# Optimization experiments

Measured on AMD Instinct MI355X. Metric: run time of the kernel, lower is better.

The kernel has to match this reference:

```python
import jax, jax.numpy as jnp
import numpy as np

N = 100000          # num nodes
E = 1600000         # num edges (before self loops)
IN_C = 128
OUT_C = 64
RATIO = 0.5
NEG_SLOPE = 0.2


def setup_inputs() -> dict:
    key = jax.random.key(0)
    k1, k2, k3, k4, k5 = jax.random.split(key, 5)
    x = jax.random.normal(k1, (N, IN_C), jnp.float32)
    # edges with no self loops (module removes then re-adds self loops)
    src = jax.random.randint(k2, (E,), 0, N, dtype=jnp.int32)
    off = jax.random.randint(k3, (E,), 1, N, dtype=jnp.int32)
    tgt = (src + off) % N
    edge_index = jnp.stack([src, tgt])  # [2, E], row0=source(j), row1=target(i)
    # glorot init
    s_w = float(np.sqrt(6.0 / (IN_C + OUT_C)))
    weight = jax.random.uniform(k4, (IN_C, OUT_C), jnp.float32, -s_w, s_w)
    s_a = float(np.sqrt(6.0 / (1 + 2 * OUT_C)))
    att = jax.random.uniform(k5, (1, 2 * OUT_C), jnp.float32, -s_a, s_a)
    batch = jnp.zeros((N,), jnp.int32)  # single graph
    return {"x": x, "weight": weight, "att": att,
            "edge_index": edge_index, "batch": batch, "bn": 0}


def reference(x, weight, att, edge_index, batch, bn):
    # add self loops (static shapes: E + N edges)
    loops = jnp.arange(N, dtype=edge_index.dtype)
    src = jnp.concatenate([edge_index[0], loops])  # edge_index_j (source)
    tgt = jnp.concatenate([edge_index[1], loops])  # edge_index_i (target)

    h = x @ weight                      # [N, OUT_C]
    x_j = h[src]                        # [E+N, OUT_C] gathered source feats
    x_i = h[tgt]

    # alpha = (cat([x_i, x_j]) * att).sum(-1)
    alpha = x_i @ att[0, :OUT_C] + x_j @ att[0, OUT_C:]   # [E+N]
    alpha = jnp.where(alpha > 0, alpha, NEG_SLOPE * alpha)  # leaky_relu

    # edge-softmax grouped by target node (every node has a self loop -> no empty segment)
    m = jax.ops.segment_max(alpha, tgt, num_segments=N)
    a = jnp.exp(alpha - m[tgt])
    denom = jax.ops.segment_sum(a, tgt, num_segments=N)
    alpha = a / (denom[tgt] + 1e-16)

    # node importance = sum of attention over outgoing edges (grouped by source)
    alpha_sum = jax.ops.segment_sum(alpha, src, num_segments=N)

    # topk node selection (ratio of all nodes; single graph)
    k = int(np.ceil(RATIO * N))
    _, topk_idx = jax.lax.top_k(alpha_sum, k)
    node_mask = jnp.zeros((N,), bool).at[topk_idx].set(True)

    # filter_dn: keep edges whose both endpoints survive; mask instead of compacting
    edge_mask = node_mask[src] & node_mask[tgt]
    alpha_m = jnp.where(edge_mask, alpha, 0.0)

    # weighted scatter-add aggregation to target nodes (aggr='add')
    out = jax.ops.segment_sum(alpha_m[:, None] * x_j, tgt, num_segments=N)  # [N, OUT_C]
    # bn flag is 0 -> BatchNorm skipped
    return out, edge_mask, node_mask
```

## Files before the change

kernel.cpp:

```cpp
#include <hip/hip_runtime.h>
#include <stdint.h>

#define IN_C 128
#define OUT_C 64
#define NEG_SLOPE 0.2f
#define RB 256
#define RBINS 512
#define STAGE 8192
#define SXP 260
#define NGH (RBINS * RB)
#define NGHS (RBINS * RBINS)

typedef unsigned int u32;
typedef unsigned long long u64;

__device__ __forceinline__ u32 fenc(float f) {
  u32 u = __float_as_uint(f);
  return (u & 0x80000000u) ? ~u : (u | 0x80000000u);
}
__device__ __forceinline__ u64 key64(float v, int i) {
  return (((u64)fenc(v)) << 32) | (u64)(0xffffffffu - (u32)i);
}

__global__ __launch_bounds__(256) void k_init(u32* hist8, u32* done, u32* sel, u32* cnt, u32 k) {
  int i = blockIdx.x * 256 + threadIdx.x;
  if (i < 2048) hist8[i] = 0u;
  if (i < 8) { done[i] = 0u; cnt[i] = 0u; }
  if (i == 0) { sel[0] = 0u; sel[1] = 0u; sel[2] = k; sel[3] = 0u; }
}

__global__ __launch_bounds__(256) void k_gemm(const float* __restrict__ x,
                                              const float* __restrict__ w,
                                              const float* __restrict__ att,
                                              float* __restrict__ h,
                                              float* __restrict__ ai, float* __restrict__ aj,
                                              int N) {
  __shared__ float sw[IN_C * OUT_C];
  __shared__ float sx[32 * SXP];
  int tid = threadIdx.x;
  int rbase = blockIdx.x * 256;

  for (int i = tid; i < (IN_C * OUT_C) / 4; i += 256)
    ((float4*)sw)[i] = ((const float4*)w)[i];

  int c0 = (tid & 7) * 8;
  int r0 = (tid >> 3) * 8;
  float acc[8][8];
#pragma unroll
  for (int i = 0; i < 8; i++)
#pragma unroll
    for (int j = 0; j < 8; j++) acc[i][j] = 0.f;

  for (int kq = 0; kq < 4; ++kq) {
    __syncthreads();
    for (int idx = tid; idx < 256 * 8; idx += 256) {
      int row = idx >> 3, j4 = idx & 7;
      int grow = rbase + row;
      float4 v = make_float4(0.f, 0.f, 0.f, 0.f);
      if (grow < N) v = *(const float4*)&x[(size_t)grow * IN_C + kq * 32 + j4 * 4];
      sx[(j4 * 4 + 0) * SXP + row] = v.x;
      sx[(j4 * 4 + 1) * SXP + row] = v.y;
      sx[(j4 * 4 + 2) * SXP + row] = v.z;
      sx[(j4 * 4 + 3) * SXP + row] = v.w;
    }
    __syncthreads();
#pragma unroll 4
    for (int kl = 0; kl < 32; ++kl) {
      int kg = kq * 32 + kl;
      float xr[8], wv[8];
      *(float4*)&xr[0] = *(const float4*)&sx[kl * SXP + r0];
      *(float4*)&xr[4] = *(const float4*)&sx[kl * SXP + r0 + 4];
      *(float4*)&wv[0] = *(const float4*)&sw[kg * OUT_C + c0];
      *(float4*)&wv[4] = *(const float4*)&sw[kg * OUT_C + c0 + 4];
#pragma unroll
      for (int i = 0; i < 8; ++i)
#pragma unroll
        for (int j = 0; j < 8; ++j)
          acc[i][j] += xr[i] * wv[j];
    }
  }

  float pi[8], pj[8];
#pragma unroll
  for (int i = 0; i < 8; ++i) { pi[i] = 0.f; pj[i] = 0.f; }
#pragma unroll
  for (int j = 0; j < 8; ++j) {
    float a0 = att[c0 + j], a1 = att[OUT_C + c0 + j];
#pragma unroll
    for (int i = 0; i < 8; ++i) {
      pi[i] += acc[i][j] * a0;
      pj[i] += acc[i][j] * a1;
    }
  }
#pragma unroll
  for (int o = 1; o < 8; o <<= 1) {
#pragma unroll
    for (int i = 0; i < 8; ++i) {
      pi[i] += __shfl_xor(pi[i], o);
      pj[i] += __shfl_xor(pj[i], o);
    }
  }
#pragma unroll
  for (int i = 0; i < 8; ++i) {
    int row = rbase + r0 + i;
    if (row < N) {
      *(float4*)&h[(size_t)row * OUT_C + c0]     = make_float4(acc[i][0], acc[i][1], acc[i][2], acc[i][3]);
      *(float4*)&h[(size_t)row * OUT_C + c0 + 4] = make_float4(acc[i][4], acc[i][5], acc[i][6], acc[i][7]);
      if ((tid & 7) == 0) { ai[row] = pi[i]; aj[row] = pj[i]; }
    }
  }
}

__global__ __launch_bounds__(256) void k_rhist_t(const int* __restrict__ tgt,
                                                 int E, int EN, int chunk, u32* __restrict__ gh) {
  __shared__ u32 lh[RBINS];
  int tid = threadIdx.x, b = blockIdx.x;
  for (int d = tid; d < RBINS; d += 256) lh[d] = 0u;
  __syncthreads();
  int lo = b * chunk, hi = min(lo + chunk, EN);
  for (int e = lo + tid; e < hi; e += 256) {
    int t = (e < E) ? tgt[e] : e - E;
    atomicAdd(&lh[((u32)t) >> 8], 1u);
  }
  __syncthreads();
  for (int d = tid; d < RBINS; d += 256) gh[d * RB + b] = lh[d];
}

__global__ __launch_bounds__(256) void k_scanA(const u32* __restrict__ in, u32* __restrict__ out,
                                               u32* __restrict__ bsum, int n) {
  __shared__ u32 s[256];
  int i = blockIdx.x * 256 + threadIdx.x;
  u32 v = (i < n) ? in[i] : 0u;
  s[threadIdx.x] = v;
  __syncthreads();
  for (int o = 1; o < 256; o <<= 1) {
    u32 t = (threadIdx.x >= (unsigned)o) ? s[threadIdx.x - o] : 0u;
    __syncthreads();
    s[threadIdx.x] += t;
    __syncthreads();
  }
  if (i < n) out[i] = s[threadIdx.x] - v;
  if (threadIdx.x == 255) bsum[blockIdx.x] = s[255];
}

__global__ __launch_bounds__(1024) void k_scanB(u32* __restrict__ bsum, int nb) {
  __shared__ u32 s[1024];
  int tid = threadIdx.x;
  u32 v = (tid < nb) ? bsum[tid] : 0u;
  s[tid] = v;
  __syncthreads();
  for (int o = 1; o < 1024; o <<= 1) {
    u32 t = (tid >= o) ? s[tid - o] : 0u;
    __syncthreads();
    s[tid] += t;
    __syncthreads();
  }
  if (tid < nb) bsum[tid] = s[tid] - v;
}

__global__ __launch_bounds__(256) void k_scanC(u32* __restrict__ out, const u32* __restrict__ bsum, int n) {
  int i = blockIdx.x * 256 + threadIdx.x;
  if (i < n) out[i] += bsum[blockIdx.x];
}

__global__ __launch_bounds__(256) void k_rscatter_t(const int* __restrict__ src, const int* __restrict__ tgt,
                                                    int E, int EN, int chunk,
                                                    const u32* __restrict__ gh, u32* __restrict__ bufB) {
  __shared__ u32 cnt[RBINS];
  int tid = threadIdx.x, b = blockIdx.x;
  for (int d = tid; d < RBINS; d += 256) cnt[d] = gh[d * RB + b];
  __syncthreads();
  int lo = b * chunk, hi = min(lo + chunk, EN);
  for (int e = lo + tid; e < hi; e += 256) {
    int s, t;
    if (e < E) { s = src[e]; t = tgt[e]; } else { s = t = e - E; }
    u32 p = atomicAdd(&cnt[((u32)t) >> 8], 1u);
    bufB[p] = (((u32)t & 255u) << 24) | (u32)s;
  }
}

__global__ __launch_bounds__(256) void k_rpass2(const u32* __restrict__ in, u32* __restrict__ out,
                                                const u32* __restrict__ gh, u32* __restrict__ ghs,
                                                u32* __restrict__ offT, int N, int EN) {
  __shared__ u32 hist[256];
  __shared__ u32 sc[256];
  __shared__ u32 lhs[RBINS];
  __shared__ u32 stage[STAGE];
  int tid = threadIdx.x, d = blockIdx.x;
  u32 start = gh[d * RB];
  u32 end = (d < RBINS - 1) ? gh[(d + 1) * RB] : (u32)EN;
  int sz = (int)(end - start);
  hist[tid] = 0u;
  for (int dd = tid; dd < RBINS; dd += 256) lhs[dd] = 0u;
  __syncthreads();
  for (u32 p = start + tid; p < end; p += 256) {
    u32 it = in[p];
    atomicAdd(&hist[it >> 24], 1u);
    atomicAdd(&lhs[(it & 0xffffffu) >> 8], 1u);
  }
  __syncthreads();
  for (int dd = tid; dd < RBINS; dd += 256) ghs[dd * RBINS + d] = lhs[dd];
  u32 hv = hist[tid];
  sc[tid] = hv;
  __syncthreads();
  for (int o = 1; o < 256; o <<= 1) {
    u32 t = (tid >= o) ? sc[tid - o] : 0u;
    __syncthreads();
    sc[tid] += t;
    __syncthreads();
  }
  u32 excl = sc[tid] - hv;
  int node = (d << 8) + tid;
  if (node < N) offT[node] = start + excl;
  if (node == 0) offT[N] = (u32)EN;
  hist[tid] = excl;
  __syncthreads();
  bool staged = (sz <= STAGE);
  for (u32 p = start + tid; p < end; p += 256) {
    u32 it = in[p];
    u32 lp = atomicAdd(&hist[it >> 24], 1u);
    if (staged) stage[lp] = it;
    else out[start + lp] = it;
  }
  __syncthreads();
  if (staged)
    for (int i = tid; i < sz; i += 256) out[start + i] = stage[i];
}

__global__ __launch_bounds__(256) void k_softmax(const u32* __restrict__ csr, const u32* __restrict__ off,
                                                 const float* __restrict__ ai, const float* __restrict__ aj,
                                                 float* __restrict__ alpha, int N) {
  int node = blockIdx.x * 16 + (threadIdx.x >> 4);
  int lane = threadIdx.x & 15;
  if (node >= N) return;
  u32 b = off[node], e2 = off[node + 1];
  float an = ai[node];
  float mx = -1e30f;
  for (u32 p = b + lane; p < e2; p += 16) {
    u32 s = csr[p] & 0xffffffu;
    float a = an + aj[s];
    a = a > 0.f ? a : NEG_SLOPE * a;
    alpha[p] = a;
    mx = fmaxf(mx, a);
  }
#pragma unroll
  for (int o = 8; o > 0; o >>= 1) mx = fmaxf(mx, __shfl_xor(mx, o));
  float sm = 0.f;
  for (u32 p = b + lane; p < e2; p += 16) {
    float v = expf(alpha[p] - mx);
    alpha[p] = v;
    sm += v;
  }
#pragma unroll
  for (int o = 8; o > 0; o >>= 1) sm += __shfl_xor(sm, o);
  float inv = 1.f / (sm + 1e-16f);
  for (u32 p = b + lane; p < e2; p += 16) alpha[p] *= inv;
}

__global__ __launch_bounds__(256) void k_rscatter_s(const u32* __restrict__ csr,
                                                    const float* __restrict__ alpha,
                                                    const u32* __restrict__ gh, const u32* __restrict__ ghs,
                                                    u64* __restrict__ bufB, int EN) {
  __shared__ u32 cnt[RBINS];
  int tid = threadIdx.x, d = blockIdx.x;
  for (int dd = tid; dd < RBINS; dd += 256) cnt[dd] = ghs[dd * RBINS + d];
  __syncthreads();
  u32 start = gh[d * RB];
  u32 end = (d < RBINS - 1) ? gh[(d + 1) * RB] : (u32)EN;
  for (u32 e = start + tid; e < end; e += 256) {
    u32 s = csr[e] & 0xffffffu;
    u32 p = atomicAdd(&cnt[s >> 8], 1u);
    bufB[p] = (((u64)(s & 255u)) << 32) | __float_as_uint(alpha[e]);
  }
}

__global__ __launch_bounds__(256) void k_asum_acc(const u64* __restrict__ bufB,
                                                  const u32* __restrict__ ghs,
                                                  float* __restrict__ asum, int N, int EN) {
  __shared__ float sums[256];
  int tid = threadIdx.x, d = blockIdx.x;
  u32 start = ghs[d * RBINS];
  u32 end = (d < RBINS - 1) ? ghs[(d + 1) * RBINS] : (u32)EN;
  sums[tid] = 0.f;
  __syncthreads();
  for (u32 p = start + tid; p < end; p += 256) {
    u64 it = bufB[p];
    atomicAdd(&sums[(u32)(it >> 32)], __uint_as_float((u32)it));
  }
  __syncthreads();
  int node = d * 256 + tid;
  if (node < N) asum[node] = sums[tid];
}

__global__ __launch_bounds__(256) void k_histpick(const float* __restrict__ asum,
                                                  const u32* __restrict__ list_in, const u32* __restrict__ cnt_in,
                                                  u32* __restrict__ list_out, u32* __restrict__ cnt_out,
                                                  u32* __restrict__ hist8, u32* __restrict__ done,
                                                  u32* __restrict__ sel, int N, int pass, int nblk) {
  __shared__ u32 lh[256];
  __shared__ u32 sres;
  __shared__ u32 s[256];
  int tid = threadIdx.x;
  lh[tid] = 0u;
  __syncthreads();
  u64 prefix = ((const u64*)sel)[0];
  int shift = 56 - 8 * pass;
  int n = list_in ? (int)*cnt_in : N;
  int i = blockIdx.x * 256 + tid;
  if (i < n) {
    int idx = list_in ? (int)list_in[i] : i;
    u64 k = key64(asum[idx], idx);
    bool ok = (pass == 0) || ((k >> (shift + 8)) == prefix);
    if (ok) {
      atomicAdd(&lh[(u32)(k >> shift) & 255u], 1u);
      if (list_out) {
        u32 p = atomicAdd(cnt_out, 1u);
        list_out[p] = (u32)idx;
      }
    }
  }
  __syncthreads();
  if (lh[tid]) atomicAdd(&hist8[pass * 256 + tid], lh[tid]);
  __syncthreads();
  if (tid == 0)
    sres = __hip_atomic_fetch_add(&done[pass], 1u, __ATOMIC_ACQ_REL, __HIP_MEMORY_SCOPE_AGENT);
  __syncthreads();
  if (sres == (u32)(nblk - 1)) {
    u32 krem = sel[2];
    u32 hv = __hip_atomic_load(&hist8[pass * 256 + (255 - tid)], __ATOMIC_RELAXED,
                               __HIP_MEMORY_SCOPE_AGENT);
    s[tid] = hv;
    __syncthreads();
    for (int o = 1; o < 256; o <<= 1) {
      u32 t = (tid >= o) ? s[tid - o] : 0u;
      __syncthreads();
      s[tid] += t;
      __syncthreads();
    }
    u32 cum = s[tid], prev = (tid > 0) ? s[tid - 1] : 0u;
    if (cum >= krem && prev < krem) {
      int dsel = 255 - tid;
      ((u64*)sel)[0] = (prefix << 8) | (u64)(u32)dsel;
      sel[2] = krem - prev;
    }
  }
}

__global__ __launch_bounds__(256) void k_finish(const float* __restrict__ asum,
                                                const u32* __restrict__ list, const u32* __restrict__ cntp,
                                                u32* __restrict__ sel) {
  __shared__ u64 keys[2048];
  __shared__ u32 cc;
  int tid = threadIdx.x;
  if (tid == 0) cc = 0u;
  __syncthreads();
  int n = (int)*cntp;
  u32 fsel = (u32)((const u64*)sel)[0];
  u32 krem = sel[2];
  for (int i = tid; i < n; i += 256) {
    int idx = (int)list[i];
    u64 k = key64(asum[idx], idx);
    if ((u32)(k >> 32) == fsel) {
      u32 p = atomicAdd(&cc, 1u);
      if (p < 2048) keys[p] = k;
    }
  }
  __syncthreads();
  int C = (int)min(cc, 2048u);
  for (int i = tid; i < C; i += 256) {
    u64 k = keys[i];
    u32 rank = 0;
    for (int j = 0; j < C; ++j)
      if (keys[j] > k) rank++;
    if (rank == krem - 1) ((u64*)sel)[0] = k;
  }
}

__global__ __launch_bounds__(256) void k_node_mask(const float* __restrict__ asum,
                                                   const u32* __restrict__ sel,
                                                   u32* __restrict__ nm,
                                                   float* __restrict__ out_node, int N) {
  int i = blockIdx.x * 256 + threadIdx.x;
  if (i >= N) return;
  u64 T = ((const u64*)sel)[0];
  bool m = key64(asum[i], i) >= T;
  nm[i] = m ? 1u : 0u;
  out_node[i] = m ? 1.f : 0.f;
}

__global__ __launch_bounds__(256) void k_mask(const int* __restrict__ src, const int* __restrict__ tgt,
                                              const u32* __restrict__ nm,
                                              const u32* __restrict__ csr, const float* __restrict__ alpha,
                                              float* __restrict__ out_edge, u64* __restrict__ pair,
                                              int E, int EN) {
  int e = blockIdx.x * 256 + threadIdx.x;
  if (e >= EN) return;
  int s, t;
  if (e < E) { s = src[e]; t = tgt[e]; } else { s = t = e - E; }
  out_edge[e] = (nm[s] && nm[t]) ? 1.f : 0.f;
  u32 sp = csr[e] & 0xffffffu;
  u32 ab = nm[sp] ? __float_as_uint(alpha[e]) : 0u;
  pair[e] = (((u64)sp) << 32) | ab;
}

__global__ __launch_bounds__(256) void k_aggregate(const u32* __restrict__ off,
                                                   const u64* __restrict__ pair,
                                                   const float* __restrict__ h,
                                                   const u32* __restrict__ nm,
                                                   float* __restrict__ out, int N) {
  int node = blockIdx.x * 4 + (threadIdx.x >> 6);
  int lane = threadIdx.x & 63;
  int g = lane >> 4;
  int c = lane & 15;
  if (node >= N) return;
  float4 acc = make_float4(0.f, 0.f, 0.f, 0.f);
  if (nm[node]) {
    u32 b = off[node], e2 = off[node + 1];
    for (u32 p0 = b; p0 < e2; p0 += 16) {
      u64 pr[4];
      float av[4];
      u32 sv[4];
#pragma unroll
      for (int q = 0; q < 4; ++q) {
        u32 p = p0 + q * 4 + (u32)g;
        bool ok = p < e2;
        pr[q] = pair[ok ? p : b];
        av[q] = ok ? __uint_as_float((u32)pr[q]) : 0.f;
        sv[q] = (u32)(pr[q] >> 32);
      }
      float4 hv[4];
#pragma unroll
      for (int q = 0; q < 4; ++q)
        hv[q] = *(const float4*)&h[(size_t)sv[q] * OUT_C + c * 4];
#pragma unroll
      for (int q = 0; q < 4; ++q) {
        acc.x += av[q] * hv[q].x;
        acc.y += av[q] * hv[q].y;
        acc.z += av[q] * hv[q].z;
        acc.w += av[q] * hv[q].w;
      }
    }
#pragma unroll
    for (int o = 16; o < 64; o <<= 1) {
      acc.x += __shfl_xor(acc.x, o);
      acc.y += __shfl_xor(acc.y, o);
      acc.z += __shfl_xor(acc.z, o);
      acc.w += __shfl_xor(acc.w, o);
    }
  }
  if (g == 0)
    *(float4*)&out[(size_t)node * OUT_C + c * 4] = acc;
}

extern "C" void kernel_launch(void* const* d_in, const int* in_sizes, int n_in,
                              void* d_out, int out_size, void* d_ws, size_t ws_size,
                              hipStream_t stream) {
  const float* x   = (const float*)d_in[0];
  const float* w   = (const float*)d_in[1];
  const float* att = (const float*)d_in[2];
  const int*   ei  = (const int*)d_in[3];

  int N = in_sizes[0] / IN_C;
  int E = in_sizes[3] / 2;
  int EN = E + N;
  const int* src = ei;
  const int* tgt = ei + E;

  float* out      = (float*)d_out;
  float* out_edge = out + (size_t)N * OUT_C;
  float* out_node = out_edge + (size_t)EN;

  char* p = (char*)d_ws;
  auto alloc = [&](size_t bytes) -> char* {
    char* r = p;
    p += (bytes + 255) & ~(size_t)255;
    return r;
  };
  float* h     = (float*)alloc((size_t)N * OUT_C * 4);
  float* ai    = (float*)alloc((size_t)N * 4);
  float* aj    = (float*)alloc((size_t)N * 4);
  u32*   bufA  = (u32*)alloc((size_t)EN * 4);
  u64*   bufB  = (u64*)alloc((size_t)EN * 8);
  float* alpha = (float*)alloc((size_t)EN * 4);
  u32*   offT  = (u32*)alloc((size_t)(N + 1) * 4);
  u32*   gh    = (u32*)alloc((size_t)NGH * 4);
  u32*   ghs   = (u32*)alloc((size_t)NGHS * 4);
  u32*   bsum  = (u32*)alloc(2048 * 4);
  float* asum  = (float*)alloc((size_t)N * 4);
  u32*   nm    = (u32*)alloc((size_t)N * 4);
  u32*   hist8 = (u32*)alloc(2048 * 4);
  u32*   done  = (u32*)alloc(8 * 4);
  u32*   cnt   = (u32*)alloc(8 * 4);
  u32*   sel   = (u32*)alloc(256);
  u32*   listA = (u32*)alloc((size_t)N * 4);
  u32*   listB = (u32*)alloc((size_t)N * 4);

  u32 kSel = (u32)((N + 1) / 2);
  int chunk = (EN + RB - 1) / RB;
  int nScanT = (NGH + 255) / 256;
  int nScanS = (NGHS + 255) / 256;
  int gRow = (N + 255) / 256;
  int gN = (N + 255) / 256;
  int gE = (EN + 255) / 256;
  int gNode4 = (N + 3) / 4;
  int gNode16 = (N + 15) / 16;

  k_init<<<8, 256, 0, stream>>>(hist8, done, sel, cnt, kSel);
  k_gemm<<<gRow, 256, 0, stream>>>(x, w, att, h, ai, aj, N);

  k_rhist_t<<<RB, 256, 0, stream>>>(tgt, E, EN, chunk, gh);
  k_scanA<<<nScanT, 256, 0, stream>>>(gh, gh, bsum, NGH);
  k_scanB<<<1, 1024, 0, stream>>>(bsum, nScanT);
  k_scanC<<<nScanT, 256, 0, stream>>>(gh, bsum, NGH);
  k_rscatter_t<<<RB, 256, 0, stream>>>(src, tgt, E, EN, chunk, gh, (u32*)bufB);
  k_rpass2<<<RBINS, 256, 0, stream>>>((u32*)bufB, bufA, gh, ghs, offT, N, EN);

  k_softmax<<<gNode16, 256, 0, stream>>>(bufA, offT, ai, aj, alpha, N);

  k_scanA<<<nScanS, 256, 0, stream>>>(ghs, ghs, bsum, NGHS);
  k_scanB<<<1, 1024, 0, stream>>>(bsum, nScanS);
  k_scanC<<<nScanS, 256, 0, stream>>>(ghs, bsum, NGHS);
  k_rscatter_s<<<RBINS, 256, 0, stream>>>(bufA, alpha, gh, ghs, bufB, EN);
  k_asum_acc<<<RBINS, 256, 0, stream>>>(bufB, ghs, asum, N, EN);

  k_histpick<<<gN, 256, 0, stream>>>(asum, nullptr, nullptr, nullptr, nullptr,
                                     hist8, done, sel, N, 0, gN);
  k_histpick<<<gN, 256, 0, stream>>>(asum, nullptr, nullptr, listA, &cnt[1],
                                     hist8, done, sel, N, 1, gN);
  k_histpick<<<gN, 256, 0, stream>>>(asum, listA, &cnt[1], listB, &cnt[2],
                                     hist8, done, sel, N, 2, gN);
  k_histpick<<<gN, 256, 0, stream>>>(asum, listB, &cnt[2], listA, &cnt[3],
                                     hist8, done, sel, N, 3, gN);
  k_finish<<<1, 256, 0, stream>>>(asum, listA, &cnt[3], sel);

  k_node_mask<<<gN, 256, 0, stream>>>(asum, sel, nm, out_node, N);
  k_mask<<<gE, 256, 0, stream>>>(src, tgt, nm, bufA, alpha, out_edge, bufB, E, EN);
  k_aggregate<<<gNode4, 256, 0, stream>>>(offT, bufB, h, nm, out, N);
}
```

Before: 376.1 us.

## Fuse edge softmax into CSR build, fold init into histogram, retile GEMM

Three changes at once. The per-target softmax now runs inside the second radix pass, with one thread per node working on the segment still held in shared memory, so the separate softmax launch and its reloads of the CSR are gone. The init kernel is folded into block 0 of the target histogram kernel. The GEMM x-tile now uses an 8-wide k-chunk with a padded row-group layout, which shrinks shared memory but adds more barriers. The fused softmax walks each segment serially in one thread, so load balance across lanes may be worse than the earlier 16-lanes-per-node version.

```diff
diff --git a/kernel.cpp b/kernel.cpp
--- a/kernel.cpp
+++ b/kernel.cpp
@@ -7,9 +7,10 @@
 #define RB 256
 #define RBINS 512
 #define STAGE 8192
-#define SXP 260
 #define NGH (RBINS * RB)
 #define NGHS (RBINS * RBINS)
+#define KC 8
+#define SXW 384
 
 typedef unsigned int u32;
 typedef unsigned long long u64;
@@ -20,13 +21,6 @@
 }
 __device__ __forceinline__ u64 key64(float v, int i) {
   return (((u64)fenc(v)) << 32) | (u64)(0xffffffffu - (u32)i);
-}
-
-__global__ __launch_bounds__(256) void k_init(u32* hist8, u32* done, u32* sel, u32* cnt, u32 k) {
-  int i = blockIdx.x * 256 + threadIdx.x;
-  if (i < 2048) hist8[i] = 0u;
-  if (i < 8) { done[i] = 0u; cnt[i] = 0u; }
-  if (i == 0) { sel[0] = 0u; sel[1] = 0u; sel[2] = k; sel[3] = 0u; }
 }
 
 __global__ __launch_bounds__(256) void k_gemm(const float* __restrict__ x,
@@ -36,7 +30,7 @@
                                               float* __restrict__ ai, float* __restrict__ aj,
                                               int N) {
   __shared__ float sw[IN_C * OUT_C];
-  __shared__ float sx[32 * SXP];
+  __shared__ float sx[KC * SXW];
   int tid = threadIdx.x;
   int rbase = blockIdx.x * 256;
 
@@ -44,32 +38,38 @@
     ((float4*)sw)[i] = ((const float4*)w)[i];
 
   int c0 = (tid & 7) * 8;
-  int r0 = (tid >> 3) * 8;
+  int rg = tid >> 3;
+  int sxbase = rg * 12;
   float acc[8][8];
 #pragma unroll
   for (int i = 0; i < 8; i++)
 #pragma unroll
     for (int j = 0; j < 8; j++) acc[i][j] = 0.f;
 
-  for (int kq = 0; kq < 4; ++kq) {
-    __syncthreads();
-    for (int idx = tid; idx < 256 * 8; idx += 256) {
-      int row = idx >> 3, j4 = idx & 7;
-      int grow = rbase + row;
+  int str = tid >> 1;
+  int skq = tid & 1;
+
+  for (int kb = 0; kb < IN_C; kb += KC) {
+    __syncthreads();
+#pragma unroll
+    for (int it = 0; it < 2; ++it) {
+      int r = str + it * 128;
+      int grow = rbase + r;
       float4 v = make_float4(0.f, 0.f, 0.f, 0.f);
-      if (grow < N) v = *(const float4*)&x[(size_t)grow * IN_C + kq * 32 + j4 * 4];
-      sx[(j4 * 4 + 0) * SXP + row] = v.x;
-      sx[(j4 * 4 + 1) * SXP + row] = v.y;
-      sx[(j4 * 4 + 2) * SXP + row] = v.z;
-      sx[(j4 * 4 + 3) * SXP + row] = v.w;
-    }
-    __syncthreads();
-#pragma unroll 4
-    for (int kl = 0; kl < 32; ++kl) {
-      int kg = kq * 32 + kl;
+      if (grow < N) v = *(const float4*)&x[(size_t)grow * IN_C + kb + skq * 4];
+      int base = (r >> 3) * 12 + (r & 7);
+      sx[(skq * 4 + 0) * SXW + base] = v.x;
+      sx[(skq * 4 + 1) * SXW + base] = v.y;
+      sx[(skq * 4 + 2) * SXW + base] = v.z;
+      sx[(skq * 4 + 3) * SXW + base] = v.w;
+    }
+    __syncthreads();
+#pragma unroll
+    for (int kl = 0; kl < KC; ++kl) {
+      int kg = kb + kl;
       float xr[8], wv[8];
-      *(float4*)&xr[0] = *(const float4*)&sx[kl * SXP + r0];
-      *(float4*)&xr[4] = *(const float4*)&sx[kl * SXP + r0 + 4];
+      *(float4*)&xr[0] = *(const float4*)&sx[kl * SXW + sxbase];
+      *(float4*)&xr[4] = *(const float4*)&sx[kl * SXW + sxbase + 4];
       *(float4*)&wv[0] = *(const float4*)&sw[kg * OUT_C + c0];
       *(float4*)&wv[4] = *(const float4*)&sw[kg * OUT_C + c0 + 4];
 #pragma unroll
@@ -102,7 +102,7 @@
   }
 #pragma unroll
   for (int i = 0; i < 8; ++i) {
-    int row = rbase + r0 + i;
+    int row = rbase + rg * 8 + i;
     if (row < N) {
       *(float4*)&h[(size_t)row * OUT_C + c0]     = make_float4(acc[i][0], acc[i][1], acc[i][2], acc[i][3]);
       *(float4*)&h[(size_t)row * OUT_C + c0 + 4] = make_float4(acc[i][4], acc[i][5], acc[i][6], acc[i][7]);
@@ -112,9 +112,16 @@
 }
 
 __global__ __launch_bounds__(256) void k_rhist_t(const int* __restrict__ tgt,
-                                                 int E, int EN, int chunk, u32* __restrict__ gh) {
+                                                 int E, int EN, int chunk, u32* __restrict__ gh,
+                                                 u32* __restrict__ hist8, u32* __restrict__ done,
+                                                 u32* __restrict__ sel, u32* __restrict__ cnt, u32 k) {
   __shared__ u32 lh[RBINS];
   int tid = threadIdx.x, b = blockIdx.x;
+  if (b == 0) {
+    for (int i = tid; i < 2048; i += 256) hist8[i] = 0u;
+    if (tid < 8) { done[tid] = 0u; cnt[tid] = 0u; }
+    if (tid == 0) { sel[0] = 0u; sel[1] = 0u; sel[2] = k; sel[3] = 0u; }
+  }
   for (int d = tid; d < RBINS; d += 256) lh[d] = 0u;
   __syncthreads();
   int lo = b * chunk, hi = min(lo + chunk, EN);
@@ -181,7 +188,10 @@
 
 __global__ __launch_bounds__(256) void k_rpass2(const u32* __restrict__ in, u32* __restrict__ out,
                                                 const u32* __restrict__ gh, u32* __restrict__ ghs,
-                                                u32* __restrict__ offT, int N, int EN) {
+                                                u32* __restrict__ offT,
+                                                const float* __restrict__ ai, const float* __restrict__ aj,
+                                                float* __restrict__ alpha,
+                                                int N, int EN) {
   __shared__ u32 hist[256];
   __shared__ u32 sc[256];
   __shared__ u32 lhs[RBINS];
@@ -225,36 +235,39 @@
   __syncthreads();
   if (staged)
     for (int i = tid; i < sz; i += 256) out[start + i] = stage[i];
-}
-
-__global__ __launch_bounds__(256) void k_softmax(const u32* __restrict__ csr, const u32* __restrict__ off,
-                                                 const float* __restrict__ ai, const float* __restrict__ aj,
-                                                 float* __restrict__ alpha, int N) {
-  int node = blockIdx.x * 16 + (threadIdx.x >> 4);
-  int lane = threadIdx.x & 15;
-  if (node >= N) return;
-  u32 b = off[node], e2 = off[node + 1];
-  float an = ai[node];
-  float mx = -1e30f;
-  for (u32 p = b + lane; p < e2; p += 16) {
-    u32 s = csr[p] & 0xffffffu;
-    float a = an + aj[s];
-    a = a > 0.f ? a : NEG_SLOPE * a;
-    alpha[p] = a;
-    mx = fmaxf(mx, a);
-  }
-#pragma unroll
-  for (int o = 8; o > 0; o >>= 1) mx = fmaxf(mx, __shfl_xor(mx, o));
-  float sm = 0.f;
-  for (u32 p = b + lane; p < e2; p += 16) {
-    float v = expf(alpha[p] - mx);
-    alpha[p] = v;
-    sm += v;
-  }
-#pragma unroll
-  for (int o = 8; o > 0; o >>= 1) sm += __shfl_xor(sm, o);
-  float inv = 1.f / (sm + 1e-16f);
-  for (u32 p = b + lane; p < e2; p += 16) alpha[p] *= inv;
+  __syncthreads();
+  if (node < N) {
+    int lb = (tid > 0) ? (int)sc[tid - 1] : 0;
+    int le = (int)sc[tid];
+    float an = ai[node];
+    float mx = -1e30f;
+    for (int i = lb; i < le; ++i) {
+      u32 it = staged ? stage[i] : out[start + i];
+      float a = an + aj[it & 0xffffffu];
+      a = a > 0.f ? a : NEG_SLOPE * a;
+      mx = fmaxf(mx, a);
+      if (staged) stage[i] = __float_as_uint(a);
+    }
+    float sm = 0.f;
+    for (int i = lb; i < le; ++i) {
+      float a;
+      if (staged) a = __uint_as_float(stage[i]);
+      else {
+        u32 it = out[start + i];
+        a = an + aj[it & 0xffffffu];
+        a = a > 0.f ? a : NEG_SLOPE * a;
+      }
+      float v = expf(a - mx);
+      sm += v;
+      if (staged) stage[i] = __float_as_uint(v);
+      else alpha[start + i] = v;
+    }
+    float inv = 1.f / (sm + 1e-16f);
+    for (int i = lb; i < le; ++i) {
+      float v = staged ? __uint_as_float(stage[i]) : alpha[start + i];
+      alpha[start + i] = v * inv;
+    }
+  }
 }
 
 __global__ __launch_bounds__(256) void k_rscatter_s(const u32* __restrict__ csr,
@@ -503,19 +516,15 @@
   int gN = (N + 255) / 256;
   int gE = (EN + 255) / 256;
   int gNode4 = (N + 3) / 4;
-  int gNode16 = (N + 15) / 16;
-
-  k_init<<<8, 256, 0, stream>>>(hist8, done, sel, cnt, kSel);
+
   k_gemm<<<gRow, 256, 0, stream>>>(x, w, att, h, ai, aj, N);
 
-  k_rhist_t<<<RB, 256, 0, stream>>>(tgt, E, EN, chunk, gh);
+  k_rhist_t<<<RB, 256, 0, stream>>>(tgt, E, EN, chunk, gh, hist8, done, sel, cnt, kSel);
   k_scanA<<<nScanT, 256, 0, stream>>>(gh, gh, bsum, NGH);
   k_scanB<<<1, 1024, 0, stream>>>(bsum, nScanT);
   k_scanC<<<nScanT, 256, 0, stream>>>(gh, bsum, NGH);
   k_rscatter_t<<<RB, 256, 0, stream>>>(src, tgt, E, EN, chunk, gh, (u32*)bufB);
-  k_rpass2<<<RBINS, 256, 0, stream>>>((u32*)bufB, bufA, gh, ghs, offT, N, EN);
-
-  k_softmax<<<gNode16, 256, 0, stream>>>(bufA, offT, ai, aj, alpha, N);
+  k_rpass2<<<RBINS, 256, 0, stream>>>((u32*)bufB, bufA, gh, ghs, offT, ai, aj, alpha, N, EN);
 
   k_scanA<<<nScanS, 256, 0, stream>>>(ghs, ghs, bsum, NGHS);
   k_scanB<<<1, 1024, 0, stream>>>(bsum, nScanS);
```

New measurement: 372.9 us. No clear change (-0.9%).
